# Optimization experiments

Hardware: AMD Instinct MI355X
Metric: run time of the kernel (lower is better)

The kernel has to match this reference:

```python
import jax, jax.numpy as jnp
import numpy as np

NEG_SLOPE = 0.2  # PyG GATConv default


def _gat_layer(x, src, dst, W, a_s, a_d, b, num_nodes):
    H, C = a_s.shape
    h = (x @ W).reshape(num_nodes, H, C)                     # [N,H,C]
    alpha_src = jnp.einsum('nhc,hc->nh', h, a_s)             # [N,H]
    alpha_dst = jnp.einsum('nhc,hc->nh', h, a_d)             # [N,H]
    e = jax.nn.leaky_relu(alpha_src[src] + alpha_dst[dst], NEG_SLOPE)  # [E,H]
    # segment softmax over incoming edges of each destination node
    m = jax.lax.stop_gradient(jax.ops.segment_max(e, dst, num_segments=num_nodes))
    e = jnp.exp(e - m[dst])
    den = jax.ops.segment_sum(e, dst, num_segments=num_nodes)
    alpha = e / den[dst]                                     # [E,H]
    msg = h[src] * alpha[:, :, None]                         # [E,H,C]
    out = jax.ops.segment_sum(msg, dst, num_segments=num_nodes)
    return out.reshape(num_nodes, H * C) + b


def setup_inputs() -> dict:
    key = jax.random.key(0)
    ks = jax.random.split(key, 10)
    N, E, D, H, C = 100000, 1600000, 128, 4, 32
    s = 1.0 / np.sqrt(D)
    return {
        'x': jax.random.normal(ks[0], (N, D), jnp.float32),
        'edge_index': jax.random.randint(ks[1], (2, E), 0, N, jnp.int64),
        'W1': jax.random.normal(ks[2], (D, H * C), jnp.float32) * s,
        'a_src1': jax.random.normal(ks[3], (H, C), jnp.float32) * s,
        'a_dst1': jax.random.normal(ks[4], (H, C), jnp.float32) * s,
        'b1': jnp.zeros((H * C,), jnp.float32),
        'W2': jax.random.normal(ks[5], (H * C, H * C), jnp.float32) * s,
        'a_src2': jax.random.normal(ks[6], (H, C), jnp.float32) * s,
        'a_dst2': jax.random.normal(ks[7], (H, C), jnp.float32) * s,
        'b2': jnp.zeros((H * C,), jnp.float32),
    }


def reference(x, edge_index, W1, a_src1, a_dst1, b1, W2, a_src2, a_dst2, b2):
    N = x.shape[0]
    loop = jnp.arange(N, dtype=edge_index.dtype)  # PyG add_self_loops=True
    src = jnp.concatenate([edge_index[0], loop])
    dst = jnp.concatenate([edge_index[1], loop])
    h = _gat_layer(x, src, dst, W1, a_src1, a_dst1, b1, N)
    h = jax.nn.relu(h)
    h = _gat_layer(h, src, dst, W2, a_src2, a_dst2, b2, N)
    return jax.nn.relu(h)
```

## Files before the change

kernel.cpp:

```cpp
#include <hip/hip_runtime.h>
#include <cstdint>
#include <cstddef>

#define NEG_SLOPE 0.2f
#define BIN_SHIFT 9
#define BCAP 16384

typedef short bf16x8 __attribute__((ext_vector_type(8)));
typedef float f32x4 __attribute__((ext_vector_type(4)));

static __device__ __forceinline__ float lrelu(float v) { return fmaxf(v, NEG_SLOPE * v); }

static __device__ __forceinline__ unsigned short bf16r(float f) {
    unsigned u = __float_as_uint(f);
    return (unsigned short)((u + 0x7fffu + ((u >> 16) & 1u)) >> 16);
}

__global__ __launch_bounds__(256) void wprep_k(const float* __restrict__ W1, const float* __restrict__ W2,
                                               unsigned short* __restrict__ Wh1, unsigned short* __restrict__ Wl1,
                                               unsigned short* __restrict__ Wh2, unsigned short* __restrict__ Wl2,
                                               int* __restrict__ bcnt) {
    if (blockIdx.x == 0) bcnt[threadIdx.x] = 0;
    int t = blockIdx.x * 256 + threadIdx.x;
    const float* W;
    unsigned short *Wh, *Wl;
    int idx;
    if (t < 16384) { W = W1; Wh = Wh1; Wl = Wl1; idx = t; }
    else           { W = W2; Wh = Wh2; Wl = Wl2; idx = t - 16384; }
    int c = idx >> 7;
    int k = idx & 127;
    float w = W[(size_t)k * 128 + c];
    unsigned short h = bf16r(w);
    float lo = w - __uint_as_float((unsigned)h << 16);
    Wh[c * 128 + k] = h;
    Wl[c * 128 + k] = bf16r(lo);
}

__global__ __launch_bounds__(256) void bin_k(const int* __restrict__ srcI, const int* __restrict__ dstI,
                                             int E, int N, int K, int* __restrict__ bcnt,
                                             int2* __restrict__ tmpE) {
    __shared__ int hist[256];
    __shared__ int lbase[256];
    const int t = threadIdx.x;
    const int M = E + N;
    const int chunk0 = blockIdx.x * 4096;
    hist[t] = 0;
    __syncthreads();

    int s[16], d[16], b[16];
#pragma unroll
    for (int j = 0; j < 16; ++j) {
        int i = chunk0 + t + j * 256;
        b[j] = -1;
        if (i < M) {
            int ss, dd;
            if (i < E) { ss = srcI[i]; dd = dstI[i]; }
            else       { ss = i - E;  dd = ss; }
            if ((unsigned)dd < (unsigned)N && (unsigned)ss < (unsigned)N) {
                s[j] = ss; d[j] = dd; b[j] = dd >> BIN_SHIFT;
                atomicAdd(&hist[b[j]], 1);
            }
        }
    }
    __syncthreads();
    if (t < K) {
        int c = hist[t];
        lbase[t] = (c > 0) ? atomicAdd(&bcnt[t], c) : 0;
    }
    hist[t] = 0;
    __syncthreads();
#pragma unroll
    for (int j = 0; j < 16; ++j) {
        if (b[j] >= 0) {
            int r = atomicAdd(&hist[b[j]], 1);
            int pos = lbase[b[j]] + r;
            if (pos < BCAP) tmpE[(size_t)b[j] * BCAP + pos] = make_int2(s[j], d[j]);
        }
    }
}

__global__ __launch_bounds__(256) void scatter_csr_k(const int2* __restrict__ tmpE,
                                                     const int* __restrict__ bcnt,
                                                     int* __restrict__ rowptr,
                                                     int* __restrict__ colSrc,
                                                     int N, int K) {
    __shared__ int pre[256];
    __shared__ int cur[512];
    __shared__ int ss[256];
    const int t = threadIdx.x;
    const int b = blockIdx.x;

    int bc = (t < K) ? min(bcnt[t], BCAP) : 0;
    pre[t] = bc;
    __syncthreads();
    for (int off = 1; off < 256; off <<= 1) {
        int v = (t >= off) ? pre[t - off] : 0;
        __syncthreads();
        pre[t] += v;
        __syncthreads();
    }
    const int base_b = (b == 0) ? 0 : pre[b - 1];
    const int cnt_b  = pre[b] - base_b;
    if (b == K - 1 && t == 0) rowptr[N] = pre[K - 1];

    const int nlo = b << BIN_SHIFT;
    const int nhi = min(nlo + (1 << BIN_SHIFT), N);
    const int nn  = nhi - nlo;
    const int2* te = tmpE + (size_t)b * BCAP;

    cur[t] = 0;
    cur[t + 256] = 0;
    __syncthreads();
    for (int i = t; i < cnt_b; i += 256) atomicAdd(&cur[te[i].y - nlo], 1);
    __syncthreads();

    int v0 = cur[2 * t], v1 = cur[2 * t + 1];
    ss[t] = v0 + v1;
    __syncthreads();
    for (int off = 1; off < 256; off <<= 1) {
        int v = (t >= off) ? ss[t - off] : 0;
        __syncthreads();
        ss[t] += v;
        __syncthreads();
    }
    int e0 = (t == 0) ? 0 : ss[t - 1];
    int e1 = e0 + v0;
    if (2 * t < nn)     rowptr[nlo + 2 * t]     = base_b + e0;
    if (2 * t + 1 < nn) rowptr[nlo + 2 * t + 1] = base_b + e1;
    cur[2 * t] = e0;
    cur[2 * t + 1] = e1;
    __syncthreads();

    for (int i = t; i < cnt_b; i += 256) {
        int2 sd = te[i];
        int r = atomicAdd(&cur[sd.y - nlo], 1);
        colSrc[base_b + r] = sd.x;
    }
}

__global__ __launch_bounds__(256) void gemm_mfma_k(const float* __restrict__ X,
                                                   const unsigned short* __restrict__ Wh,
                                                   const unsigned short* __restrict__ Wl,
                                                   const float* __restrict__ a_s,
                                                   const float* __restrict__ a_d,
                                                   unsigned short* __restrict__ Hout,
                                                   float* __restrict__ asrc,
                                                   float* __restrict__ adst,
                                                   int N) {
    __shared__ __align__(16) unsigned short hstage[4][32][132];
    const int tid = threadIdx.x;
    const int wid = tid >> 6;
    const int l   = tid & 63;
    const int l15 = l & 15;
    const int lh  = l >> 4;
    const int waveRow = blockIdx.x * 128 + wid * 32;
    if (waveRow >= N) return;

    f32x4 acc[2][8];
#pragma unroll
    for (int m = 0; m < 2; ++m)
#pragma unroll
        for (int f = 0; f < 8; ++f)
#pragma unroll
            for (int c = 0; c < 4; ++c) acc[m][f][c] = 0.f;

    const int r0 = waveRow + l15;
    const int r1 = waveRow + 16 + l15;
    const size_t xoff0 = (size_t)min(r0, N - 1) * 128;
    const size_t xoff1 = (size_t)min(r1, N - 1) * 128;
    const int kb = lh * 8;

#pragma unroll
    for (int ks = 0; ks < 4; ++ks) {
        bf16x8 ah[2], al[2];
#pragma unroll
        for (int m = 0; m < 2; ++m) {
            const float* xp = X + (m ? xoff1 : xoff0) + ks * 32 + kb;
            float4 v0 = *(const float4*)xp;
            float4 v1 = *(const float4*)(xp + 4);
            float xs[8] = {v0.x, v0.y, v0.z, v0.w, v1.x, v1.y, v1.z, v1.w};
#pragma unroll
            for (int j = 0; j < 8; ++j) {
                unsigned short h = bf16r(xs[j]);
                float hf = __uint_as_float((unsigned)h << 16);
                ah[m][j] = (short)h;
                al[m][j] = (short)bf16r(xs[j] - hf);
            }
        }
        const unsigned short* wb  = Wh + (size_t)l15 * 128 + ks * 32 + kb;
        const unsigned short* wbl = Wl + (size_t)l15 * 128 + ks * 32 + kb;
#pragma unroll
        for (int f = 0; f < 8; ++f) {
            bf16x8 wh = *(const bf16x8*)(wb + f * 2048);
            bf16x8 wl = *(const bf16x8*)(wbl + f * 2048);
#pragma unroll
            for (int m = 0; m < 2; ++m) {
                acc[m][f] = __builtin_amdgcn_mfma_f32_16x16x32_bf16(ah[m], wh, acc[m][f], 0, 0, 0);
                acc[m][f] = __builtin_amdgcn_mfma_f32_16x16x32_bf16(al[m], wh, acc[m][f], 0, 0, 0);
                acc[m][f] = __builtin_amdgcn_mfma_f32_16x16x32_bf16(ah[m], wl, acc[m][f], 0, 0, 0);
            }
        }
    }

    float asf[8], adf[8];
#pragma unroll
    for (int f = 0; f < 8; ++f) {
        asf[f] = a_s[f * 16 + l15];
        adf[f] = a_d[f * 16 + l15];
    }
    const int q = l15;
#pragma unroll
    for (int m = 0; m < 2; ++m) {
#pragma unroll
        for (int r = 0; r < 4; ++r) {
            float ps[4] = {0.f, 0.f, 0.f, 0.f};
            float pd[4] = {0.f, 0.f, 0.f, 0.f};
#pragma unroll
            for (int f = 0; f < 8; ++f) {
                float v = acc[m][f][r];
                ps[f >> 1] = fmaf(v, asf[f], ps[f >> 1]);
                pd[f >> 1] = fmaf(v, adf[f], pd[f >> 1]);
                hstage[wid][m * 16 + lh * 4 + r][f * 16 + l15] = bf16r(v);
            }
#pragma unroll
            for (int mask = 1; mask < 16; mask <<= 1) {
#pragma unroll
                for (int h = 0; h < 4; ++h) {
                    ps[h] += __shfl_xor(ps[h], mask);
                    pd[h] += __shfl_xor(pd[h], mask);
                }
            }
            int row = waveRow + m * 16 + lh * 4 + r;
            if (q < 8 && row < N) {
                float v0 = (q & 1) ? ps[1] : ps[0];
                float v1 = (q & 1) ? ps[3] : ps[2];
                float vs = (q & 2) ? v1 : v0;
                float w0 = (q & 1) ? pd[1] : pd[0];
                float w1 = (q & 1) ? pd[3] : pd[2];
                float vd = (q & 2) ? w1 : w0;
                if (q < 4) asrc[row * 4 + q] = vs;
                else       adst[row * 4 + (q - 4)] = vd;
            }
        }
    }

#pragma unroll
    for (int it = 0; it < 8; ++it) {
        int row = it * 4 + lh;
        const unsigned short* hp = &hstage[wid][row][l15 * 8];
        uint2 aa = *(const uint2*)hp;
        uint2 bb = *(const uint2*)(hp + 4);
        int grow = waveRow + row;
        if (grow < N) {
            uint4 o;
            o.x = aa.x; o.y = aa.y; o.z = bb.x; o.w = bb.y;
            *(uint4*)&Hout[(size_t)grow * 128 + l15 * 8] = o;
        }
    }
}

__global__ __launch_bounds__(256) void aggregate_k(const unsigned short* __restrict__ Hbuf,
                                                   const float* __restrict__ asrc,
                                                   const float* __restrict__ adst,
                                                   const int* __restrict__ rowptr,
                                                   const int* __restrict__ colSrc,
                                                   const float* __restrict__ bias,
                                                   float* __restrict__ out, int N) {
    int wave = (blockIdx.x * 256 + threadIdx.x) >> 6;
    int lane = threadIdx.x & 63;
    if (wave >= N) return;
    const int n = wave;
    const int c0 = lane * 2;
    const int head = c0 >> 5;
    const float adh = adst[n * 4 + head];
    int b = __builtin_amdgcn_readfirstlane(rowptr[n]);
    int e = __builtin_amdgcn_readfirstlane(rowptr[n + 1]);
    float acc0 = 0.f, acc1 = 0.f, sw = 0.f;
    int p = b;
    for (; p + 8 <= e; p += 8) {
        int s[8];
#pragma unroll
        for (int j = 0; j < 8; ++j) s[j] = colSrc[p + j];
        float a[8];
#pragma unroll
        for (int j = 0; j < 8; ++j) a[j] = asrc[s[j] * 4 + head];
        unsigned hu[8];
#pragma unroll
        for (int j = 0; j < 8; ++j) hu[j] = *(const unsigned*)&Hbuf[(size_t)s[j] * 128 + c0];
#pragma unroll
        for (int j = 0; j < 8; ++j) {
            float w = __expf(lrelu(a[j] + adh));
            sw += w;
            acc0 = fmaf(w, __uint_as_float(hu[j] << 16), acc0);
            acc1 = fmaf(w, __uint_as_float(hu[j] & 0xffff0000u), acc1);
        }
    }
    for (; p < e; ++p) {
        int s = colSrc[p];
        float w = __expf(lrelu(asrc[s * 4 + head] + adh));
        unsigned u = *(const unsigned*)&Hbuf[(size_t)s * 128 + c0];
        sw += w;
        acc0 = fmaf(w, __uint_as_float(u << 16), acc0);
        acc1 = fmaf(w, __uint_as_float(u & 0xffff0000u), acc1);
    }
    float inv_dh = 1.f / sw;
    float o0 = fmaxf(acc0 * inv_dh + bias[c0], 0.f);
    float o1 = fmaxf(acc1 * inv_dh + bias[c0 + 1], 0.f);
    *(float2*)&out[(size_t)n * 128 + c0] = make_float2(o0, o1);
}


extern "C" void kernel_launch(void* const* d_in, const int* in_sizes, int n_in,
                              void* d_out, int out_size, void* d_ws, size_t ws_size,
                              hipStream_t stream) {
    const float* X   = (const float*)d_in[0];
    const int*   EI  = (const int*)d_in[1];
    const float* W1  = (const float*)d_in[2];
    const float* as1 = (const float*)d_in[3];
    const float* ad1 = (const float*)d_in[4];
    const float* b1  = (const float*)d_in[5];
    const float* W2  = (const float*)d_in[6];
    const float* as2 = (const float*)d_in[7];
    const float* ad2 = (const float*)d_in[8];
    const float* b2  = (const float*)d_in[9];

    const int N = in_sizes[0] / 128;
    const int E = in_sizes[1] / 2;
    const int M = E + N;
    const int K = (N + (1 << BIN_SHIFT) - 1) >> BIN_SHIFT;
    const int* srcI = EI;
    const int* dstI = EI + E;

    char* w = (char*)d_ws;
    auto alloc = [&](size_t bytes) {
        char* p = w;
        w += (bytes + 255) & ~(size_t)255;
        return p;
    };
    unsigned short* Hbuf = (unsigned short*)alloc((size_t)N * 128 * 2);
    float* asrc   = (float*)alloc((size_t)N * 4 * 4);
    float* adst   = (float*)alloc((size_t)N * 4 * 4);
    int*   rowptr = (int*)alloc((size_t)(N + 1) * 4);
    int*   colSrc = (int*)alloc((size_t)M * 4);
    int2*  tmpE   = (int2*)alloc((size_t)K * BCAP * 8);
    int*   bcnt   = (int*)alloc(256 * 4);
    unsigned short* Wt1h = (unsigned short*)alloc(128 * 128 * 2);
    unsigned short* Wt1l = (unsigned short*)alloc(128 * 128 * 2);
    unsigned short* Wt2h = (unsigned short*)alloc(128 * 128 * 2);
    unsigned short* Wt2l = (unsigned short*)alloc(128 * 128 * 2);

    wprep_k<<<128, 256, 0, stream>>>(W1, W2, Wt1h, Wt1l, Wt2h, Wt2l, bcnt);
    bin_k<<<(M + 4095) / 4096, 256, 0, stream>>>(srcI, dstI, E, N, K, bcnt, tmpE);
    scatter_csr_k<<<K, 256, 0, stream>>>(tmpE, bcnt, rowptr, colSrc, N, K);

    float* out = (float*)d_out;

    gemm_mfma_k<<<(N + 127) / 128, 256, 0, stream>>>(X, Wt1h, Wt1l, as1, ad1, Hbuf, asrc, adst, N);
    aggregate_k<<<((size_t)N * 64 + 255) / 256, 256, 0, stream>>>(Hbuf, asrc, adst, rowptr, colSrc, b1, out, N);
    gemm_mfma_k<<<(N + 127) / 128, 256, 0, stream>>>(out, Wt2h, Wt2l, as2, ad2, Hbuf, asrc, adst, N);
    aggregate_k<<<((size_t)N * 64 + 255) / 256, 256, 0, stream>>>(Hbuf, asrc, adst, rowptr, colSrc, b2, out, N);
}
```

Baseline: 409.3 us.

## Fuse layer-1 GEMM with edge binning and restructure aggregation gather

Merges the first-layer GEMM and the edge-binning pass into one launch with block-index dispatch, so the two independent stages can run concurrently and one launch is saved. The CSR now stores byte offsets (src<<8) so aggregation indexes H and asrc without multiplies. Attention logits are pre-scaled by log2(e) in the GEMM epilogue so the softmax uses a hardware exp2. The aggregation kernel splits each wave into two half-waves that each handle alternate edges with 8-byte loads, then combines them with a cross-lane shuffle. The max-free softmax is kept; the shift limits source indices to about 8M, and the fused kernel's shared-memory footprint grows.

```diff
diff --git a/kernel.cpp b/kernel.cpp
--- a/kernel.cpp
+++ b/kernel.cpp
@@ -5,16 +5,23 @@
 #define NEG_SLOPE 0.2f
 #define BIN_SHIFT 9
 #define BCAP 16384
+#define LOG2E 1.4426950408889634f
 
 typedef short bf16x8 __attribute__((ext_vector_type(8)));
 typedef float f32x4 __attribute__((ext_vector_type(4)));
 
-static __device__ __forceinline__ float lrelu(float v) { return fmaxf(v, NEG_SLOPE * v); }
+#if __has_builtin(__builtin_amdgcn_exp2f)
+#define EXP2(x) __builtin_amdgcn_exp2f(x)
+#else
+#define EXP2(x) exp2f(x)
+#endif
 
 static __device__ __forceinline__ unsigned short bf16r(float f) {
     unsigned u = __float_as_uint(f);
     return (unsigned short)((u + 0x7fffu + ((u >> 16) & 1u)) >> 16);
 }
+static __device__ __forceinline__ float bfu_lo(unsigned u) { return __uint_as_float(u << 16); }
+static __device__ __forceinline__ float bfu_hi(unsigned u) { return __uint_as_float(u & 0xffff0000u); }
 
 __global__ __launch_bounds__(256) void wprep_k(const float* __restrict__ W1, const float* __restrict__ W2,
                                                unsigned short* __restrict__ Wh1, unsigned short* __restrict__ Wl1,
@@ -36,14 +43,12 @@
     Wl[c * 128 + k] = bf16r(lo);
 }
 
-__global__ __launch_bounds__(256) void bin_k(const int* __restrict__ srcI, const int* __restrict__ dstI,
-                                             int E, int N, int K, int* __restrict__ bcnt,
-                                             int2* __restrict__ tmpE) {
-    __shared__ int hist[256];
-    __shared__ int lbase[256];
+static __device__ void bin_body(int bid, const int* __restrict__ srcI, const int* __restrict__ dstI,
+                                int E, int N, int K, int* __restrict__ bcnt, int2* __restrict__ tmpE,
+                                int* hist, int* lbase) {
     const int t = threadIdx.x;
     const int M = E + N;
-    const int chunk0 = blockIdx.x * 4096;
+    const int chunk0 = bid * 4096;
     hist[t] = 0;
     __syncthreads();
 
@@ -82,7 +87,7 @@
 __global__ __launch_bounds__(256) void scatter_csr_k(const int2* __restrict__ tmpE,
                                                      const int* __restrict__ bcnt,
                                                      int* __restrict__ rowptr,
-                                                     int* __restrict__ colSrc,
+                                                     int* __restrict__ colOff,
                                                      int N, int K) {
     __shared__ int pre[256];
     __shared__ int cur[512];
@@ -134,7 +139,150 @@
     for (int i = t; i < cnt_b; i += 256) {
         int2 sd = te[i];
         int r = atomicAdd(&cur[sd.y - nlo], 1);
-        colSrc[base_b + r] = sd.x;
+        colOff[base_b + r] = sd.x << 8;
+    }
+}
+
+static __device__ void gemm_body(int bid, const float* __restrict__ X,
+                                 const unsigned short* __restrict__ Wh,
+                                 const unsigned short* __restrict__ Wl,
+                                 const float* __restrict__ a_s,
+                                 const float* __restrict__ a_d,
+                                 unsigned short* __restrict__ Hout,
+                                 float* __restrict__ asrc,
+                                 float* __restrict__ adst,
+                                 int N, unsigned short* hstage) {
+    const int tid = threadIdx.x;
+    const int wid = tid >> 6;
+    const int l   = tid & 63;
+    const int l15 = l & 15;
+    const int lh  = l >> 4;
+    const int waveRow = bid * 128 + wid * 32;
+    if (waveRow >= N) return;
+
+    f32x4 acc[2][8];
+#pragma unroll
+    for (int m = 0; m < 2; ++m)
+#pragma unroll
+        for (int f = 0; f < 8; ++f)
+#pragma unroll
+            for (int c = 0; c < 4; ++c) acc[m][f][c] = 0.f;
+
+    const int r0 = waveRow + l15;
+    const int r1 = waveRow + 16 + l15;
+    const size_t xoff0 = (size_t)min(r0, N - 1) * 128;
+    const size_t xoff1 = (size_t)min(r1, N - 1) * 128;
+    const int kb = lh * 8;
+
+#pragma unroll
+    for (int ks = 0; ks < 4; ++ks) {
+        bf16x8 ah[2], al[2];
+#pragma unroll
+        for (int m = 0; m < 2; ++m) {
+            const float* xp = X + (m ? xoff1 : xoff0) + ks * 32 + kb;
+            float4 v0 = *(const float4*)xp;
+            float4 v1 = *(const float4*)(xp + 4);
+            float xs[8] = {v0.x, v0.y, v0.z, v0.w, v1.x, v1.y, v1.z, v1.w};
+#pragma unroll
+            for (int j = 0; j < 8; ++j) {
+                unsigned short h = bf16r(xs[j]);
+                float hf = __uint_as_float((unsigned)h << 16);
+                ah[m][j] = (short)h;
+                al[m][j] = (short)bf16r(xs[j] - hf);
+            }
+        }
+        const unsigned short* wb  = Wh + (size_t)l15 * 128 + ks * 32 + kb;
+        const unsigned short* wbl = Wl + (size_t)l15 * 128 + ks * 32 + kb;
+#pragma unroll
+        for (int f = 0; f < 8; ++f) {
+            bf16x8 wh = *(const bf16x8*)(wb + f * 2048);
+            bf16x8 wl = *(const bf16x8*)(wbl + f * 2048);
+#pragma unroll
+            for (int m = 0; m < 2; ++m) {
+                acc[m][f] = __builtin_amdgcn_mfma_f32_16x16x32_bf16(ah[m], wh, acc[m][f], 0, 0, 0);
+                acc[m][f] = __builtin_amdgcn_mfma_f32_16x16x32_bf16(al[m], wh, acc[m][f], 0, 0, 0);
+                acc[m][f] = __builtin_amdgcn_mfma_f32_16x16x32_bf16(ah[m], wl, acc[m][f], 0, 0, 0);
+            }
+        }
+    }
+
+    float asf[8], adf[8];
+#pragma unroll
+    for (int f = 0; f < 8; ++f) {
+        asf[f] = a_s[f * 16 + l15];
+        adf[f] = a_d[f * 16 + l15];
+    }
+    const int q = l15;
+#pragma unroll
+    for (int m = 0; m < 2; ++m) {
+#pragma unroll
+        for (int r = 0; r < 4; ++r) {
+            float ps[4] = {0.f, 0.f, 0.f, 0.f};
+            float pd[4] = {0.f, 0.f, 0.f, 0.f};
+#pragma unroll
+            for (int f = 0; f < 8; ++f) {
+                float v = acc[m][f][r];
+                ps[f >> 1] = fmaf(v, asf[f], ps[f >> 1]);
+                pd[f >> 1] = fmaf(v, adf[f], pd[f >> 1]);
+                hstage[((wid * 32) + m * 16 + lh * 4 + r) * 132 + f * 16 + l15] = bf16r(v);
+            }
+#pragma unroll
+            for (int mask = 1; mask < 16; mask <<= 1) {
+#pragma unroll
+                for (int h = 0; h < 4; ++h) {
+                    ps[h] += __shfl_xor(ps[h], mask);
+                    pd[h] += __shfl_xor(pd[h], mask);
+                }
+            }
+            int row = waveRow + m * 16 + lh * 4 + r;
+            if (q < 8 && row < N) {
+                float v0 = (q & 1) ? ps[1] : ps[0];
+                float v1 = (q & 1) ? ps[3] : ps[2];
+                float vs = (q & 2) ? v1 : v0;
+                float w0 = (q & 1) ? pd[1] : pd[0];
+                float w1 = (q & 1) ? pd[3] : pd[2];
+                float vd = (q & 2) ? w1 : w0;
+                if (q < 4) asrc[row * 4 + q] = vs * LOG2E;
+                else       adst[row * 4 + (q - 4)] = vd * LOG2E;
+            }
+        }
+    }
+
+#pragma unroll
+    for (int it = 0; it < 8; ++it) {
+        int row = it * 4 + lh;
+        const unsigned short* hp = hstage + ((wid * 32) + row) * 132 + l15 * 8;
+        uint2 aa = *(const uint2*)hp;
+        uint2 bb = *(const uint2*)(hp + 4);
+        int grow = waveRow + row;
+        if (grow < N) {
+            uint4 o;
+            o.x = aa.x; o.y = aa.y; o.z = bb.x; o.w = bb.y;
+            *(uint4*)&Hout[(size_t)grow * 128 + l15 * 8] = o;
+        }
+    }
+}
+
+__global__ __launch_bounds__(256) void gemm1_bin_k(const float* __restrict__ X,
+                                                   const unsigned short* __restrict__ Wh,
+                                                   const unsigned short* __restrict__ Wl,
+                                                   const float* __restrict__ a_s,
+                                                   const float* __restrict__ a_d,
+                                                   unsigned short* __restrict__ Hout,
+                                                   float* __restrict__ asrc,
+                                                   float* __restrict__ adst,
+                                                   int N, int gemmBlocks,
+                                                   const int* __restrict__ srcI, const int* __restrict__ dstI,
+                                                   int E, int K, int* __restrict__ bcnt,
+                                                   int2* __restrict__ tmpE) {
+    __shared__ __align__(16) unsigned short hstage[4 * 32 * 132];
+    __shared__ int hist[256];
+    __shared__ int lbase[256];
+    int bid = blockIdx.x;
+    if (bid < gemmBlocks) {
+        gemm_body(bid, X, Wh, Wl, a_s, a_d, Hout, asrc, adst, N, hstage);
+    } else {
+        bin_body(bid - gemmBlocks, srcI, dstI, E, N, K, bcnt, tmpE, hist, lbase);
     }
 }
 
@@ -147,166 +295,86 @@
                                                    float* __restrict__ asrc,
                                                    float* __restrict__ adst,
                                                    int N) {
-    __shared__ __align__(16) unsigned short hstage[4][32][132];
-    const int tid = threadIdx.x;
-    const int wid = tid >> 6;
-    const int l   = tid & 63;
-    const int l15 = l & 15;
-    const int lh  = l >> 4;
-    const int waveRow = blockIdx.x * 128 + wid * 32;
-    if (waveRow >= N) return;
-
-    f32x4 acc[2][8];
-#pragma unroll
-    for (int m = 0; m < 2; ++m)
-#pragma unroll
-        for (int f = 0; f < 8; ++f)
-#pragma unroll
-            for (int c = 0; c < 4; ++c) acc[m][f][c] = 0.f;
-
-    const int r0 = waveRow + l15;
-    const int r1 = waveRow + 16 + l15;
-    const size_t xoff0 = (size_t)min(r0, N - 1) * 128;
-    const size_t xoff1 = (size_t)min(r1, N - 1) * 128;
-    const int kb = lh * 8;
-
-#pragma unroll
-    for (int ks = 0; ks < 4; ++ks) {
-        bf16x8 ah[2], al[2];
-#pragma unroll
-        for (int m = 0; m < 2; ++m) {
-            const float* xp = X + (m ? xoff1 : xoff0) + ks * 32 + kb;
-            float4 v0 = *(const float4*)xp;
-            float4 v1 = *(const float4*)(xp + 4);
-            float xs[8] = {v0.x, v0.y, v0.z, v0.w, v1.x, v1.y, v1.z, v1.w};
-#pragma unroll
-            for (int j = 0; j < 8; ++j) {
-                unsigned short h = bf16r(xs[j]);
-                float hf = __uint_as_float((unsigned)h << 16);
-                ah[m][j] = (short)h;
-                al[m][j] = (short)bf16r(xs[j] - hf);
-            }
-        }
-        const unsigned short* wb  = Wh + (size_t)l15 * 128 + ks * 32 + kb;
-        const unsigned short* wbl = Wl + (size_t)l15 * 128 + ks * 32 + kb;
-#pragma unroll
-        for (int f = 0; f < 8; ++f) {
-            bf16x8 wh = *(const bf16x8*)(wb + f * 2048);
-            bf16x8 wl = *(const bf16x8*)(wbl + f * 2048);
-#pragma unroll
-            for (int m = 0; m < 2; ++m) {
-                acc[m][f] = __builtin_amdgcn_mfma_f32_16x16x32_bf16(ah[m], wh, acc[m][f], 0, 0, 0);
-                acc[m][f] = __builtin_amdgcn_mfma_f32_16x16x32_bf16(al[m], wh, acc[m][f], 0, 0, 0);
-                acc[m][f] = __builtin_amdgcn_mfma_f32_16x16x32_bf16(ah[m], wl, acc[m][f], 0, 0, 0);
-            }
-        }
-    }
-
-    float asf[8], adf[8];
-#pragma unroll
-    for (int f = 0; f < 8; ++f) {
-        asf[f] = a_s[f * 16 + l15];
-        adf[f] = a_d[f * 16 + l15];
-    }
-    const int q = l15;
-#pragma unroll
-    for (int m = 0; m < 2; ++m) {
-#pragma unroll
-        for (int r = 0; r < 4; ++r) {
-            float ps[4] = {0.f, 0.f, 0.f, 0.f};
-            float pd[4] = {0.f, 0.f, 0.f, 0.f};
-#pragma unroll
-            for (int f = 0; f < 8; ++f) {
-                float v = acc[m][f][r];
-                ps[f >> 1] = fmaf(v, asf[f], ps[f >> 1]);
-                pd[f >> 1] = fmaf(v, adf[f], pd[f >> 1]);
-                hstage[wid][m * 16 + lh * 4 + r][f * 16 + l15] = bf16r(v);
-            }
-#pragma unroll
-            for (int mask = 1; mask < 16; mask <<= 1) {
-#pragma unroll
-                for (int h = 0; h < 4; ++h) {
-                    ps[h] += __shfl_xor(ps[h], mask);
-                    pd[h] += __shfl_xor(pd[h], mask);
-                }
-            }
-            int row = waveRow + m * 16 + lh * 4 + r;
-            if (q < 8 && row < N) {
-                float v0 = (q & 1) ? ps[1] : ps[0];
-                float v1 = (q & 1) ? ps[3] : ps[2];
-                float vs = (q & 2) ? v1 : v0;
-                float w0 = (q & 1) ? pd[1] : pd[0];
-                float w1 = (q & 1) ? pd[3] : pd[2];
-                float vd = (q & 2) ? w1 : w0;
-                if (q < 4) asrc[row * 4 + q] = vs;
-                else       adst[row * 4 + (q - 4)] = vd;
-            }
-        }
-    }
-
-#pragma unroll
-    for (int it = 0; it < 8; ++it) {
-        int row = it * 4 + lh;
-        const unsigned short* hp = &hstage[wid][row][l15 * 8];
-        uint2 aa = *(const uint2*)hp;
-        uint2 bb = *(const uint2*)(hp + 4);
-        int grow = waveRow + row;
-        if (grow < N) {
-            uint4 o;
-            o.x = aa.x; o.y = aa.y; o.z = bb.x; o.w = bb.y;
-            *(uint4*)&Hout[(size_t)grow * 128 + l15 * 8] = o;
-        }
-    }
+    __shared__ __align__(16) unsigned short hstage[4 * 32 * 132];
+    gemm_body(blockIdx.x, X, Wh, Wl, a_s, a_d, Hout, asrc, adst, N, hstage);
 }
 
 __global__ __launch_bounds__(256) void aggregate_k(const unsigned short* __restrict__ Hbuf,
                                                    const float* __restrict__ asrc,
                                                    const float* __restrict__ adst,
                                                    const int* __restrict__ rowptr,
-                                                   const int* __restrict__ colSrc,
+                                                   const int* __restrict__ colOff,
                                                    const float* __restrict__ bias,
                                                    float* __restrict__ out, int N) {
     int wave = (blockIdx.x * 256 + threadIdx.x) >> 6;
     int lane = threadIdx.x & 63;
     if (wave >= N) return;
     const int n = wave;
-    const int c0 = lane * 2;
-    const int head = c0 >> 5;
+    const int li = lane & 31;
+    const int hl = lane >> 5;
+    const int head = li >> 3;
     const float adh = adst[n * 4 + head];
+    const char* Hb = (const char*)Hbuf;
+    const char* As = (const char*)asrc;
+    const int hboff = li * 8;
+    const int aoff = head * 4;
+
     int b = __builtin_amdgcn_readfirstlane(rowptr[n]);
     int e = __builtin_amdgcn_readfirstlane(rowptr[n + 1]);
-    float acc0 = 0.f, acc1 = 0.f, sw = 0.f;
+    float a0 = 0.f, a1 = 0.f, a2 = 0.f, a3 = 0.f, sw = 0.f;
     int p = b;
     for (; p + 8 <= e; p += 8) {
-        int s[8];
-#pragma unroll
-        for (int j = 0; j < 8; ++j) s[j] = colSrc[p + j];
-        float a[8];
-#pragma unroll
-        for (int j = 0; j < 8; ++j) a[j] = asrc[s[j] * 4 + head];
-        unsigned hu[8];
-#pragma unroll
-        for (int j = 0; j < 8; ++j) hu[j] = *(const unsigned*)&Hbuf[(size_t)s[j] * 128 + c0];
-#pragma unroll
-        for (int j = 0; j < 8; ++j) {
-            float w = __expf(lrelu(a[j] + adh));
+        int off[4]; float av[4]; uint2 hu[4];
+#pragma unroll
+        for (int j = 0; j < 4; ++j) off[j] = colOff[p + 2 * j + hl];
+#pragma unroll
+        for (int j = 0; j < 4; ++j) av[j] = *(const float*)(As + (off[j] >> 4) + aoff);
+#pragma unroll
+        for (int j = 0; j < 4; ++j) hu[j] = *(const uint2*)(Hb + off[j] + hboff);
+#pragma unroll
+        for (int j = 0; j < 4; ++j) {
+            float x = av[j] + adh;
+            float w = EXP2(fmaxf(x, NEG_SLOPE * x));
             sw += w;
-            acc0 = fmaf(w, __uint_as_float(hu[j] << 16), acc0);
-            acc1 = fmaf(w, __uint_as_float(hu[j] & 0xffff0000u), acc1);
-        }
-    }
-    for (; p < e; ++p) {
-        int s = colSrc[p];
-        float w = __expf(lrelu(asrc[s * 4 + head] + adh));
-        unsigned u = *(const unsigned*)&Hbuf[(size_t)s * 128 + c0];
-        sw += w;
-        acc0 = fmaf(w, __uint_as_float(u << 16), acc0);
-        acc1 = fmaf(w, __uint_as_float(u & 0xffff0000u), acc1);
-    }
-    float inv_dh = 1.f / sw;
-    float o0 = fmaxf(acc0 * inv_dh + bias[c0], 0.f);
-    float o1 = fmaxf(acc1 * inv_dh + bias[c0 + 1], 0.f);
-    *(float2*)&out[(size_t)n * 128 + c0] = make_float2(o0, o1);
+            a0 = fmaf(w, bfu_lo(hu[j].x), a0);
+            a1 = fmaf(w, bfu_hi(hu[j].x), a1);
+            a2 = fmaf(w, bfu_lo(hu[j].y), a2);
+            a3 = fmaf(w, bfu_hi(hu[j].y), a3);
+        }
+    }
+    if (p < e) {
+#pragma unroll
+        for (int j = 0; j < 4; ++j) {
+            int q = p + 2 * j + hl;
+            bool valid = q < e;
+            int off = colOff[valid ? q : b];
+            float a = *(const float*)(As + (off >> 4) + aoff);
+            uint2 hu = *(const uint2*)(Hb + off + hboff);
+            float x = a + adh;
+            float w = valid ? EXP2(fmaxf(x, NEG_SLOPE * x)) : 0.f;
+            sw += w;
+            a0 = fmaf(w, bfu_lo(hu.x), a0);
+            a1 = fmaf(w, bfu_hi(hu.x), a1);
+            a2 = fmaf(w, bfu_lo(hu.y), a2);
+            a3 = fmaf(w, bfu_hi(hu.y), a3);
+        }
+    }
+    sw += __shfl_xor(sw, 32);
+    a0 += __shfl_xor(a0, 32);
+    a1 += __shfl_xor(a1, 32);
+    a2 += __shfl_xor(a2, 32);
+    a3 += __shfl_xor(a3, 32);
+    if (hl == 0) {
+        float inv = 1.f / sw;
+        int c0 = li * 4;
+        float4 bv = *(const float4*)&bias[c0];
+        float4 o;
+        o.x = fmaxf(a0 * inv + bv.x, 0.f);
+        o.y = fmaxf(a1 * inv + bv.y, 0.f);
+        o.z = fmaxf(a2 * inv + bv.z, 0.f);
+        o.w = fmaxf(a3 * inv + bv.w, 0.f);
+        *(float4*)&out[(size_t)n * 128 + c0] = o;
+    }
 }
 
 
@@ -341,7 +409,7 @@
     float* asrc   = (float*)alloc((size_t)N * 4 * 4);
     float* adst   = (float*)alloc((size_t)N * 4 * 4);
     int*   rowptr = (int*)alloc((size_t)(N + 1) * 4);
-    int*   colSrc = (int*)alloc((size_t)M * 4);
+    int*   colOff = (int*)alloc((size_t)M * 4);
     int2*  tmpE   = (int2*)alloc((size_t)K * BCAP * 8);
     int*   bcnt   = (int*)alloc(256 * 4);
     unsigned short* Wt1h = (unsigned short*)alloc(128 * 128 * 2);
@@ -349,14 +417,17 @@
     unsigned short* Wt2h = (unsigned short*)alloc(128 * 128 * 2);
     unsigned short* Wt2l = (unsigned short*)alloc(128 * 128 * 2);
 
+    const int gemmBlocks = (N + 127) / 128;
+    const int binBlocks  = (M + 4095) / 4096;
+
     wprep_k<<<128, 256, 0, stream>>>(W1, W2, Wt1h, Wt1l, Wt2h, Wt2l, bcnt);
-    bin_k<<<(M + 4095) / 4096, 256, 0, stream>>>(srcI, dstI, E, N, K, bcnt, tmpE);
-    scatter_csr_k<<<K, 256, 0, stream>>>(tmpE, bcnt, rowptr, colSrc, N, K);
+    gemm1_bin_k<<<gemmBlocks + binBlocks, 256, 0, stream>>>(X, Wt1h, Wt1l, as1, ad1, Hbuf, asrc, adst,
+                                                            N, gemmBlocks, srcI, dstI, E, K, bcnt, tmpE);
+    scatter_csr_k<<<K, 256, 0, stream>>>(tmpE, bcnt, rowptr, colOff, N, K);
 
     float* out = (float*)d_out;
 
-    gemm_mfma_k<<<(N + 127) / 128, 256, 0, stream>>>(X, Wt1h, Wt1l, as1, ad1, Hbuf, asrc, adst, N);
-    aggregate_k<<<((size_t)N * 64 + 255) / 256, 256, 0, stream>>>(Hbuf, asrc, adst, rowptr, colSrc, b1, out, N);
-    gemm_mfma_k<<<(N + 127) / 128, 256, 0, stream>>>(out, Wt2h, Wt2l, as2, ad2, Hbuf, asrc, adst, N);
-    aggregate_k<<<((size_t)N * 64 + 255) / 256, 256, 0, stream>>>(Hbuf, asrc, adst, rowptr, colSrc, b2, out, N);
-}
+    aggregate_k<<<((size_t)N * 64 + 255) / 256, 256, 0, stream>>>(Hbuf, asrc, adst, rowptr, colOff, b1, out, N);
+    gemm_mfma_k<<<gemmBlocks, 256, 0, stream>>>(out, Wt2h, Wt2l, as2, ad2, Hbuf, asrc, adst, N);
+    aggregate_k<<<((size_t)N * 64 + 255) / 256, 256, 0, stream>>>(Hbuf, asrc, adst, rowptr, colOff, b2, out, N);
+}
```

Result: slower. 460.6 us (+12.5%).

## Pack source attention logits into padded H rows and store byte offsets in CSR

Applied to the files above, without the earlier changes.

The per-node bf16 feature row and its four source-attention logits are stored together in one padded 272-byte record, so each gathered edge reads a single row instead of two separate arrays. The CSR column array now holds precomputed byte offsets, and the logits are prescaled by log2(e) so the softmax uses a hardware exp2. The binning kernel also handles half as many edges per block, giving twice as many blocks. The padded rows use more memory, and storing src*272 as a 32-bit int limits how many nodes can be indexed.

```diff
diff --git a/kernel.cpp b/kernel.cpp
--- a/kernel.cpp
+++ b/kernel.cpp
@@ -5,16 +5,24 @@
 #define NEG_SLOPE 0.2f
 #define BIN_SHIFT 9
 #define BCAP 16384
+#define LOG2E 1.4426950408889634f
+#define ROWB 272
 
 typedef short bf16x8 __attribute__((ext_vector_type(8)));
 typedef float f32x4 __attribute__((ext_vector_type(4)));
 
-static __device__ __forceinline__ float lrelu(float v) { return fmaxf(v, NEG_SLOPE * v); }
+#if __has_builtin(__builtin_amdgcn_exp2f)
+#define EXP2(x) __builtin_amdgcn_exp2f(x)
+#else
+#define EXP2(x) exp2f(x)
+#endif
 
 static __device__ __forceinline__ unsigned short bf16r(float f) {
     unsigned u = __float_as_uint(f);
     return (unsigned short)((u + 0x7fffu + ((u >> 16) & 1u)) >> 16);
 }
+static __device__ __forceinline__ float bfu_lo(unsigned u) { return __uint_as_float(u << 16); }
+static __device__ __forceinline__ float bfu_hi(unsigned u) { return __uint_as_float(u & 0xffff0000u); }
 
 __global__ __launch_bounds__(256) void wprep_k(const float* __restrict__ W1, const float* __restrict__ W2,
                                                unsigned short* __restrict__ Wh1, unsigned short* __restrict__ Wl1,
@@ -43,13 +51,13 @@
     __shared__ int lbase[256];
     const int t = threadIdx.x;
     const int M = E + N;
-    const int chunk0 = blockIdx.x * 4096;
+    const int chunk0 = blockIdx.x * 2048;
     hist[t] = 0;
     __syncthreads();
 
-    int s[16], d[16], b[16];
-#pragma unroll
-    for (int j = 0; j < 16; ++j) {
+    int s[8], d[8], b[8];
+#pragma unroll
+    for (int j = 0; j < 8; ++j) {
         int i = chunk0 + t + j * 256;
         b[j] = -1;
         if (i < M) {
@@ -70,7 +78,7 @@
     hist[t] = 0;
     __syncthreads();
 #pragma unroll
-    for (int j = 0; j < 16; ++j) {
+    for (int j = 0; j < 8; ++j) {
         if (b[j] >= 0) {
             int r = atomicAdd(&hist[b[j]], 1);
             int pos = lbase[b[j]] + r;
@@ -82,7 +90,7 @@
 __global__ __launch_bounds__(256) void scatter_csr_k(const int2* __restrict__ tmpE,
                                                      const int* __restrict__ bcnt,
                                                      int* __restrict__ rowptr,
-                                                     int* __restrict__ colSrc,
+                                                     int* __restrict__ colOff,
                                                      int N, int K) {
     __shared__ int pre[256];
     __shared__ int cur[512];
@@ -134,7 +142,7 @@
     for (int i = t; i < cnt_b; i += 256) {
         int2 sd = te[i];
         int r = atomicAdd(&cur[sd.y - nlo], 1);
-        colSrc[base_b + r] = sd.x;
+        colOff[base_b + r] = sd.x * ROWB;
     }
 }
 
@@ -143,8 +151,7 @@
                                                    const unsigned short* __restrict__ Wl,
                                                    const float* __restrict__ a_s,
                                                    const float* __restrict__ a_d,
-                                                   unsigned short* __restrict__ Hout,
-                                                   float* __restrict__ asrc,
+                                                   char* __restrict__ Hout,
                                                    float* __restrict__ adst,
                                                    int N) {
     __shared__ __align__(16) unsigned short hstage[4][32][132];
@@ -238,8 +245,8 @@
                 float w0 = (q & 1) ? pd[1] : pd[0];
                 float w1 = (q & 1) ? pd[3] : pd[2];
                 float vd = (q & 2) ? w1 : w0;
-                if (q < 4) asrc[row * 4 + q] = vs;
-                else       adst[row * 4 + (q - 4)] = vd;
+                if (q < 4) *(float*)(Hout + (size_t)row * ROWB + 256 + q * 4) = vs * LOG2E;
+                else       adst[row * 4 + (q - 4)] = vd * LOG2E;
             }
         }
     }
@@ -254,16 +261,15 @@
         if (grow < N) {
             uint4 o;
             o.x = aa.x; o.y = aa.y; o.z = bb.x; o.w = bb.y;
-            *(uint4*)&Hout[(size_t)grow * 128 + l15 * 8] = o;
-        }
-    }
-}
-
-__global__ __launch_bounds__(256) void aggregate_k(const unsigned short* __restrict__ Hbuf,
-                                                   const float* __restrict__ asrc,
+            *(uint4*)(Hout + (size_t)grow * ROWB + l15 * 16) = o;
+        }
+    }
+}
+
+__global__ __launch_bounds__(256) void aggregate_k(const char* __restrict__ Hb,
                                                    const float* __restrict__ adst,
                                                    const int* __restrict__ rowptr,
-                                                   const int* __restrict__ colSrc,
+                                                   const int* __restrict__ colOff,
                                                    const float* __restrict__ bias,
                                                    float* __restrict__ out, int N) {
     int wave = (blockIdx.x * 256 + threadIdx.x) >> 6;
@@ -273,39 +279,44 @@
     const int c0 = lane * 2;
     const int head = c0 >> 5;
     const float adh = adst[n * 4 + head];
+    const int hoff = c0 * 2;
+    const int aoff = 256 + head * 4;
+
     int b = __builtin_amdgcn_readfirstlane(rowptr[n]);
     int e = __builtin_amdgcn_readfirstlane(rowptr[n + 1]);
     float acc0 = 0.f, acc1 = 0.f, sw = 0.f;
     int p = b;
     for (; p + 8 <= e; p += 8) {
-        int s[8];
-#pragma unroll
-        for (int j = 0; j < 8; ++j) s[j] = colSrc[p + j];
+        int off[8];
+#pragma unroll
+        for (int j = 0; j < 8; ++j) off[j] = colOff[p + j];
         float a[8];
 #pragma unroll
-        for (int j = 0; j < 8; ++j) a[j] = asrc[s[j] * 4 + head];
+        for (int j = 0; j < 8; ++j) a[j] = *(const float*)(Hb + off[j] + aoff);
         unsigned hu[8];
 #pragma unroll
-        for (int j = 0; j < 8; ++j) hu[j] = *(const unsigned*)&Hbuf[(size_t)s[j] * 128 + c0];
+        for (int j = 0; j < 8; ++j) hu[j] = *(const unsigned*)(Hb + off[j] + hoff);
 #pragma unroll
         for (int j = 0; j < 8; ++j) {
-            float w = __expf(lrelu(a[j] + adh));
+            float x = a[j] + adh;
+            float w = EXP2(fmaxf(x, NEG_SLOPE * x));
             sw += w;
-            acc0 = fmaf(w, __uint_as_float(hu[j] << 16), acc0);
-            acc1 = fmaf(w, __uint_as_float(hu[j] & 0xffff0000u), acc1);
+            acc0 = fmaf(w, bfu_lo(hu[j]), acc0);
+            acc1 = fmaf(w, bfu_hi(hu[j]), acc1);
         }
     }
     for (; p < e; ++p) {
-        int s = colSrc[p];
-        float w = __expf(lrelu(asrc[s * 4 + head] + adh));
-        unsigned u = *(const unsigned*)&Hbuf[(size_t)s * 128 + c0];
+        int off = colOff[p];
+        float x = *(const float*)(Hb + off + aoff) + adh;
+        unsigned u = *(const unsigned*)(Hb + off + hoff);
+        float w = EXP2(fmaxf(x, NEG_SLOPE * x));
         sw += w;
-        acc0 = fmaf(w, __uint_as_float(u << 16), acc0);
-        acc1 = fmaf(w, __uint_as_float(u & 0xffff0000u), acc1);
-    }
-    float inv_dh = 1.f / sw;
-    float o0 = fmaxf(acc0 * inv_dh + bias[c0], 0.f);
-    float o1 = fmaxf(acc1 * inv_dh + bias[c0 + 1], 0.f);
+        acc0 = fmaf(w, bfu_lo(u), acc0);
+        acc1 = fmaf(w, bfu_hi(u), acc1);
+    }
+    float inv = 1.f / sw;
+    float o0 = fmaxf(acc0 * inv + bias[c0], 0.f);
+    float o1 = fmaxf(acc1 * inv + bias[c0 + 1], 0.f);
     *(float2*)&out[(size_t)n * 128 + c0] = make_float2(o0, o1);
 }
 
@@ -337,11 +348,10 @@
         w += (bytes + 255) & ~(size_t)255;
         return p;
     };
-    unsigned short* Hbuf = (unsigned short*)alloc((size_t)N * 128 * 2);
-    float* asrc   = (float*)alloc((size_t)N * 4 * 4);
+    char*  Hbuf   = (char*)alloc((size_t)N * ROWB);
     float* adst   = (float*)alloc((size_t)N * 4 * 4);
     int*   rowptr = (int*)alloc((size_t)(N + 1) * 4);
-    int*   colSrc = (int*)alloc((size_t)M * 4);
+    int*   colOff = (int*)alloc((size_t)M * 4);
     int2*  tmpE   = (int2*)alloc((size_t)K * BCAP * 8);
     int*   bcnt   = (int*)alloc(256 * 4);
     unsigned short* Wt1h = (unsigned short*)alloc(128 * 128 * 2);
@@ -349,14 +359,16 @@
     unsigned short* Wt2h = (unsigned short*)alloc(128 * 128 * 2);
     unsigned short* Wt2l = (unsigned short*)alloc(128 * 128 * 2);
 
+    const int gemmBlocks = (N + 127) / 128;
+
     wprep_k<<<128, 256, 0, stream>>>(W1, W2, Wt1h, Wt1l, Wt2h, Wt2l, bcnt);
-    bin_k<<<(M + 4095) / 4096, 256, 0, stream>>>(srcI, dstI, E, N, K, bcnt, tmpE);
-    scatter_csr_k<<<K, 256, 0, stream>>>(tmpE, bcnt, rowptr, colSrc, N, K);
+    bin_k<<<(M + 2047) / 2048, 256, 0, stream>>>(srcI, dstI, E, N, K, bcnt, tmpE);
+    scatter_csr_k<<<K, 256, 0, stream>>>(tmpE, bcnt, rowptr, colOff, N, K);
 
     float* out = (float*)d_out;
 
-    gemm_mfma_k<<<(N + 127) / 128, 256, 0, stream>>>(X, Wt1h, Wt1l, as1, ad1, Hbuf, asrc, adst, N);
-    aggregate_k<<<((size_t)N * 64 + 255) / 256, 256, 0, stream>>>(Hbuf, asrc, adst, rowptr, colSrc, b1, out, N);
-    gemm_mfma_k<<<(N + 127) / 128, 256, 0, stream>>>(out, Wt2h, Wt2l, as2, ad2, Hbuf, asrc, adst, N);
-    aggregate_k<<<((size_t)N * 64 + 255) / 256, 256, 0, stream>>>(Hbuf, asrc, adst, rowptr, colSrc, b2, out, N);
-}
+    gemm_mfma_k<<<gemmBlocks, 256, 0, stream>>>(X, Wt1h, Wt1l, as1, ad1, Hbuf, adst, N);
+    aggregate_k<<<((size_t)N * 64 + 255) / 256, 256, 0, stream>>>(Hbuf, adst, rowptr, colOff, b1, out, N);
+    gemm_mfma_k<<<gemmBlocks, 256, 0, stream>>>(out, Wt2h, Wt2l, as2, ad2, Hbuf, adst, N);
+    aggregate_k<<<((size_t)N * 64 + 255) / 256, 256, 0, stream>>>(Hbuf, adst, rowptr, colOff, b2, out, N);
+}
```

New measurement: 425.5 us. 4.0% more time.
